# Kernel tuning notes

Measured on AMD Instinct MI355X. Metric: run time of the kernel, lower is better.

The kernel has to match this reference:

```python
import jax, jax.numpy as jnp
import numpy as np

N_NODES = 100000
N_EDGES = 3200000
IN_DIM, HID_DIM, OUT_DIM = 512, 256, 64


def setup_inputs() -> dict:
    key = jax.random.key(0)
    k1, k2, k3, k4, k5, k6 = jax.random.split(key, 6)
    x = jax.random.normal(k1, (N_NODES, IN_DIM), dtype=jnp.float32)
    src = jax.random.randint(k2, (N_EDGES,), 0, N_NODES, dtype=jnp.int32)
    dst = jax.random.randint(k3, (N_EDGES,), 0, N_NODES, dtype=jnp.int32)
    edge_index = jnp.stack([src, dst])  # [2, E]: row 0 = src (column), row 1 = dst (row)
    edge_weight = jax.random.uniform(k4, (N_EDGES,), dtype=jnp.float32)
    # Xavier-uniform init like nn.init.xavier_uniform_
    lim1 = float(np.sqrt(6.0 / (IN_DIM + HID_DIM)))
    lim2 = float(np.sqrt(6.0 / (HID_DIM + OUT_DIM)))
    W1 = jax.random.uniform(k5, (IN_DIM, HID_DIM), minval=-lim1, maxval=lim1, dtype=jnp.float32)
    W2 = jax.random.uniform(k6, (HID_DIM, OUT_DIM), minval=-lim2, maxval=lim2, dtype=jnp.float32)
    return {"x": x, "edge_index": edge_index, "edge_weight": edge_weight, "W1": W1, "W2": W2}


def _spmm(edge_index, edge_weight, support):
    # out[dst] += w * support[src]  (sparse adjacency @ dense support)
    src, dst = edge_index[0], edge_index[1]
    msgs = support[src] * edge_weight[:, None]  # [E, F]
    return jax.ops.segment_sum(msgs, dst, num_segments=N_NODES)


def reference(x, edge_index, edge_weight, W1, W2):
    # Layer 1: dense GEMM then SpMM, then ReLU (dropout is identity in eval)
    h = _spmm(edge_index, edge_weight, x @ W1)
    h = jax.nn.relu(h)
    # Layer 2
    out = _spmm(edge_index, edge_weight, h @ W2)
    return jax.nn.softmax(out, axis=1)
```

## Files before the change

### kernel.cpp

```cpp
#include <hip/hip_runtime.h>
#include <hip/hip_bf16.h>

typedef __attribute__((ext_vector_type(8))) short bf16x8;
typedef __attribute__((ext_vector_type(4))) float f32x4;
typedef __attribute__((ext_vector_type(8))) float f32x8;
typedef __attribute__((ext_vector_type(4))) _Float16 f16x4;
typedef __attribute__((ext_vector_type(8))) _Float16 f16x8;
typedef unsigned short ushort_t;

#define NN   100000
#define NE   3200000
#define IND  512
#define HIDD 256
#define OUTD 64

#define NBKT 98
#define P1E  2048
#define MPAN 782

__device__ __forceinline__ ushort_t f2bf(float a) {
    unsigned u = __float_as_uint(a);
    unsigned r = (u + 0x7FFFu + ((u >> 16) & 1u)) >> 16;
    return (ushort_t)r;
}
__device__ __forceinline__ float bf2f(ushort_t b) {
    return __uint_as_float(((unsigned)b) << 16);
}

union U8 { ushort_t us[8]; unsigned u32[4]; uint4 v; };

#define GLOAD_LDS16(gp, lp) \
    __builtin_amdgcn_global_load_lds( \
        (const __attribute__((address_space(1))) void*)(const void*)(gp), \
        (__attribute__((address_space(3))) void*)(void*)(lp), 16, 0, 0)

__device__ __forceinline__ void split8(float4 v0, float4 v1, bf16x8& aH, bf16x8& aL) {
    float vv[8] = {v0.x, v0.y, v0.z, v0.w, v1.x, v1.y, v1.z, v1.w};
    U8 H, L;
    #pragma unroll
    for (int j = 0; j < 4; ++j) {
        unsigned u0 = __float_as_uint(vv[2 * j]);
        unsigned u1 = __float_as_uint(vv[2 * j + 1]);
        H.u32[j] = __builtin_amdgcn_perm(u1, u0, 0x07060302u);
        float r0 = vv[2 * j]     - __uint_as_float(u0 & 0xFFFF0000u);
        float r1 = vv[2 * j + 1] - __uint_as_float(u1 & 0xFFFF0000u);
        L.u32[j] = __builtin_amdgcn_perm(__float_as_uint(r1),
                                         __float_as_uint(r0), 0x07060302u);
    }
    aH = *(const bf16x8*)&H.v;
    aL = *(const bf16x8*)&L.v;
}

__global__ void splitw_k(const float* __restrict__ in, ushort_t* __restrict__ thi,
                         ushort_t* __restrict__ tlo, int R, int C) {
    int i = blockIdx.x * 256 + threadIdx.x;
    if (i < R * C) {
        int r = i / C, c = i % C;
        float a = in[i];
        ushort_t h = f2bf(a);
        thi[(size_t)c * R + r] = h;
        tlo[(size_t)c * R + r] = f2bf(a - bf2f(h));
    }
}

__global__ __launch_bounds__(256, 3) void gemm1_k(
    const float* __restrict__ A, const ushort_t* __restrict__ BtHi,
    const ushort_t* __restrict__ BtLo, _Float16* __restrict__ C)
{
    const int M = NN, N = HIDD, K = IND;
    __shared__ __align__(16) float    sA [128 * 32];
    __shared__ __align__(16) ushort_t sBh[128 * 32];
    __shared__ __align__(16) ushort_t sBl[128 * 32];

    const int bid   = blockIdx.x;
    const int grp   = bid >> 4;
    const int rr_   = bid & 15;
    const int panel = grp * 8 + (rr_ & 7);
    if (panel >= MPAN) return;
    const int m0 = panel * 128;
    const int n0 = (rr_ >> 3) * 128;

    const int tid  = threadIdx.x;
    const int wave = tid >> 6;
    const int lane = tid & 63;
    const int quad = lane >> 4;
    const int l15  = lane & 15;
    const int wr   = wave >> 1;
    const int wc   = wave & 1;

    const float* aSrc[4];
    float*       aDst[4];
    #pragma unroll
    for (int it = 0; it < 4; ++it) {
        int f = it * 256 + tid;
        int r = f >> 3;
        int bp = (f & 7) ^ ((r & 3) << 1) ^ ((r >> 2) & 1);
        int gr = m0 + r; if (gr >= M) gr = M - 1;
        aSrc[it] = A + (size_t)gr * K + bp * 4;
        aDst[it] = &sA[f * 4];
    }
    const ushort_t* bhSrc[2]; const ushort_t* blSrc[2];
    ushort_t* bhDst[2]; ushort_t* blDst[2];
    #pragma unroll
    for (int it = 0; it < 2; ++it) {
        int f = it * 256 + tid;
        int r = f >> 2;
        int qp = (f & 3) ^ ((r >> 1) & 3);
        bhSrc[it] = BtHi + (size_t)(n0 + r) * K + qp * 8;
        blSrc[it] = BtLo + (size_t)(n0 + r) * K + qp * 8;
        bhDst[it] = &sBh[f * 8];
        blDst[it] = &sBl[f * 8];
    }

    int aOff[4][2];
    #pragma unroll
    for (int ms = 0; ms < 4; ++ms) {
        int rA = wr * 64 + ms * 16 + l15;
        int sw = ((rA & 3) << 1) ^ ((rA >> 2) & 1);
        int cb = quad << 1;
        aOff[ms][0] = rA * 32 + (((cb    ) ^ sw) << 2);
        aOff[ms][1] = rA * 32 + (((cb | 1) ^ sw) << 2);
    }
    int bOff[4];
    #pragma unroll
    for (int ns = 0; ns < 4; ++ns) {
        int rB = wc * 64 + ns * 16 + l15;
        bOff[ns] = rB * 32 + (quad ^ ((rB >> 1) & 3)) * 8;
    }

    f32x4 acc[4][4] = {};

    for (int k0 = 0; k0 < K; k0 += 32) {
        #pragma unroll
        for (int it = 0; it < 4; ++it) GLOAD_LDS16(aSrc[it] + k0, aDst[it]);
        #pragma unroll
        for (int it = 0; it < 2; ++it) {
            GLOAD_LDS16(bhSrc[it] + k0, bhDst[it]);
            GLOAD_LDS16(blSrc[it] + k0, blDst[it]);
        }
        __syncthreads();

        bf16x8 aH[4], aL[4];
        #pragma unroll
        for (int ms = 0; ms < 4; ++ms) {
            float4 v0 = *(const float4*)&sA[aOff[ms][0]];
            float4 v1 = *(const float4*)&sA[aOff[ms][1]];
            split8(v0, v1, aH[ms], aL[ms]);
        }

        #pragma unroll
        for (int ns = 0; ns < 4; ++ns) {
            bf16x8 bH = *(const bf16x8*)&sBh[bOff[ns]];
            bf16x8 bL = *(const bf16x8*)&sBl[bOff[ns]];
            #pragma unroll
            for (int ms = 0; ms < 4; ++ms) {
                acc[ms][ns] = __builtin_amdgcn_mfma_f32_16x16x32_bf16(aH[ms], bH, acc[ms][ns], 0, 0, 0);
                acc[ms][ns] = __builtin_amdgcn_mfma_f32_16x16x32_bf16(aL[ms], bH, acc[ms][ns], 0, 0, 0);
                acc[ms][ns] = __builtin_amdgcn_mfma_f32_16x16x32_bf16(aH[ms], bL, acc[ms][ns], 0, 0, 0);
            }
        }
        __syncthreads();
    }

    #pragma unroll
    for (int ms = 0; ms < 4; ++ms) {
        int row = m0 + wr * 64 + ms * 16 + quad * 4;
        #pragma unroll
        for (int ns = 0; ns < 4; ++ns) {
            int col = n0 + wc * 64 + ns * 16 + l15;
            #pragma unroll
            for (int r = 0; r < 4; ++r)
                if (row + r < M) C[(size_t)(row + r) * N + col] = (_Float16)acc[ms][ns][r];
        }
    }
}

__global__ __launch_bounds__(256) void bhist_k(const int* __restrict__ dst,
                                               int* __restrict__ bucketHist) {
    __shared__ int h[NBKT];
    int t = threadIdx.x;
    if (t < NBKT) h[t] = 0;
    __syncthreads();
    #pragma unroll
    for (int j = 0; j < 4; ++j) {
        int e = blockIdx.x * 1024 + t + j * 256;
        if (e < NE) atomicAdd(&h[dst[e] >> 10], 1);
    }
    __syncthreads();
    if (t < NBKT && h[t]) atomicAdd(&bucketHist[t], h[t]);
}

__global__ __launch_bounds__(128) void bscan_k(const int* __restrict__ bucketHist,
                                               int* __restrict__ bucketStart,
                                               int* __restrict__ bucketCursor) {
    __shared__ int s[128];
    int t = threadIdx.x;
    int v = (t < NBKT) ? bucketHist[t] : 0;
    s[t] = v;
    for (int off = 1; off < 128; off <<= 1) {
        __syncthreads();
        int a = (t >= off) ? s[t - off] : 0;
        __syncthreads();
        s[t] += a;
    }
    __syncthreads();
    if (t < NBKT) { bucketStart[t] = s[t] - v; bucketCursor[t] = s[t] - v; }
    if (t == NBKT - 1) bucketStart[NBKT] = s[t];
}

__global__ __launch_bounds__(256) void phase1_k(
    const int* __restrict__ src, const int* __restrict__ dst,
    const float* __restrict__ w, int* __restrict__ bucketCursor,
    int2* __restrict__ binned)
{
    __shared__ int2 raw[P1E];
    __shared__ int2 ord[P1E];
    __shared__ ushort_t rbkt[P1E], obkt[P1E];
    __shared__ int hist[128], excl[128], cursor[128], gbase[128], stmp[128];

    int t = threadIdx.x;
    if (t < 128) hist[t] = 0;
    __syncthreads();

    int e0 = blockIdx.x * P1E;
    #pragma unroll
    for (int j = 0; j < P1E / 256; ++j) {
        int li = t + j * 256;
        int e = e0 + li;
        if (e < NE) {
            int d = dst[e];
            int b = d >> 10;
            raw[li] = make_int2(src[e] | ((d & 1023) << 17), __float_as_int(w[e]));
            rbkt[li] = (ushort_t)b;
            atomicAdd(&hist[b], 1);
        } else rbkt[li] = 0xFFFFu;
    }
    __syncthreads();
    int v = (t < 128) ? hist[t] : 0;
    if (t < 128) stmp[t] = v;
    for (int off = 1; off < 128; off <<= 1) {
        __syncthreads();
        int a = (t < 128 && t >= off) ? stmp[t - off] : 0;
        __syncthreads();
        if (t < 128) stmp[t] += a;
    }
    __syncthreads();
    if (t < 128) { excl[t] = stmp[t] - v; cursor[t] = stmp[t] - v; }
    if (t < NBKT) gbase[t] = atomicAdd(&bucketCursor[t], hist[t]);
    __syncthreads();
    #pragma unroll
    for (int j = 0; j < P1E / 256; ++j) {
        int li = t + j * 256;
        ushort_t b = rbkt[li];
        if (b != 0xFFFFu) {
            int p = atomicAdd(&cursor[b], 1);
            ord[p] = raw[li];
            obkt[p] = b;
        }
    }
    __syncthreads();
    int tot = excl[NBKT - 1] + hist[NBKT - 1];
    #pragma unroll
    for (int j = 0; j < P1E / 256; ++j) {
        int li = t + j * 256;
        if (li < tot) {
            int b = obkt[li];
            binned[(size_t)gbase[b] + (li - excl[b])] = ord[li];
        }
    }
}

__global__ __launch_bounds__(256) void phase2_k(
    const int* __restrict__ bucketStart, const int2* __restrict__ binned,
    int* __restrict__ rowptr, int2* __restrict__ esw)
{
    __shared__ int cnt[1024], ex[1024], cur[1024], wsum[256];
    int t = threadIdx.x, blk = blockIdx.x;
    int gb = bucketStart[blk], ge = bucketStart[blk + 1];
    #pragma unroll
    for (int j = 0; j < 4; ++j) cnt[t + j * 256] = 0;
    __syncthreads();
    for (int e = gb + t; e < ge; e += 256)
        atomicAdd(&cnt[(binned[e].x >> 17) & 1023], 1);
    __syncthreads();
    int b4 = t * 4;
    int l0 = cnt[b4], l1 = cnt[b4 + 1], l2 = cnt[b4 + 2], l3 = cnt[b4 + 3];
    int ls = l0 + l1 + l2 + l3;
    wsum[t] = ls;
    for (int off = 1; off < 256; off <<= 1) {
        __syncthreads();
        int a = (t >= off) ? wsum[t - off] : 0;
        __syncthreads();
        wsum[t] += a;
    }
    __syncthreads();
    int be = wsum[t] - ls;
    ex[b4] = be;            cur[b4] = be;
    ex[b4 + 1] = be + l0;     cur[b4 + 1] = be + l0;
    ex[b4 + 2] = be + l0 + l1;  cur[b4 + 2] = be + l0 + l1;
    ex[b4 + 3] = be + l0 + l1 + l2; cur[b4 + 3] = be + l0 + l1 + l2;
    __syncthreads();
    int n0 = blk << 10;
    #pragma unroll
    for (int j = 0; j < 4; ++j) {
        int i = b4 + j;
        if (n0 + i < NN) rowptr[n0 + i] = gb + ex[i];
    }
    if (blk == NBKT - 1 && t == 0) rowptr[NN] = NE;
    for (int e = gb + t; e < ge; e += 256) {
        int2 en = binned[e];
        int d = (en.x >> 17) & 1023;
        int p = atomicAdd(&cur[d], 1);
        esw[(size_t)gb + p] = make_int2(en.x & 0x1FFFF, en.y);
    }
}

__global__ __launch_bounds__(256) void spmm_relu_gemm2_k(
    const int* __restrict__ rowptr, const int2* __restrict__ esw,
    const _Float16* __restrict__ X, const ushort_t* __restrict__ BtHi,
    const ushort_t* __restrict__ BtLo, _Float16* __restrict__ S2)
{
    __shared__ __align__(16) float h[16][260];

    const int wave  = threadIdx.x >> 6;
    const int lane  = threadIdx.x & 63;
    const int quad  = lane >> 4;
    const int l15   = lane & 15;
    const int half  = lane >> 5;
    const int l31   = lane & 31;
    const int nbase = blockIdx.x * 16;

    const _Float16* Xl = X + l31 * 8;
    #pragma unroll
    for (int i = 0; i < 4; ++i) {
        const int ln   = wave * 4 + i;
        const int node = nbase + ln;
        const int beg = rowptr[node], end = rowptr[node + 1];
        f32x8 acc = {0.f, 0.f, 0.f, 0.f, 0.f, 0.f, 0.f, 0.f};
        int e = beg;
        #pragma unroll 4
        for (; e + 1 < end; e += 2) {
            int2 sw = esw[e + half];
            float w = __int_as_float(sw.y);
            f16x8 v = *(const f16x8*)(Xl + (size_t)sw.x * HIDD);
            #pragma unroll
            for (int j = 0; j < 8; ++j) acc[j] += (float)v[j] * w;
        }
        if (e < end) {
            int2 sw = esw[e];
            float w = half ? 0.f : __int_as_float(sw.y);
            f16x8 v = *(const f16x8*)(Xl + (size_t)sw.x * HIDD);
            #pragma unroll
            for (int j = 0; j < 8; ++j) acc[j] += (float)v[j] * w;
        }
        #pragma unroll
        for (int j = 0; j < 8; ++j) acc[j] += __shfl_xor(acc[j], 32);
        if (half == 0) {
            float4 r0, r1;
            r0.x = fmaxf(acc[0], 0.f); r0.y = fmaxf(acc[1], 0.f);
            r0.z = fmaxf(acc[2], 0.f); r0.w = fmaxf(acc[3], 0.f);
            r1.x = fmaxf(acc[4], 0.f); r1.y = fmaxf(acc[5], 0.f);
            r1.z = fmaxf(acc[6], 0.f); r1.w = fmaxf(acc[7], 0.f);
            *(float4*)&h[ln][l31 * 8]     = r0;
            *(float4*)&h[ln][l31 * 8 + 4] = r1;
        }
    }
    __syncthreads();

    f32x4 acc2 = {0.f, 0.f, 0.f, 0.f};
    const ushort_t* bh = BtHi + (size_t)(wave * 16 + l15) * HIDD;
    const ushort_t* bl = BtLo + (size_t)(wave * 16 + l15) * HIDD;
    #pragma unroll
    for (int ks = 0; ks < 8; ++ks) {
        const int ko = ks * 32 + quad * 8;
        const float* ap = &h[l15][ko];
        float4 v0 = *(const float4*)ap;
        float4 v1 = *(const float4*)(ap + 4);
        bf16x8 aH, aL;
        split8(v0, v1, aH, aL);
        bf16x8 bH = *(const bf16x8*)(bh + ko);
        bf16x8 bL = *(const bf16x8*)(bl + ko);
        acc2 = __builtin_amdgcn_mfma_f32_16x16x32_bf16(aH, bH, acc2, 0, 0, 0);
        acc2 = __builtin_amdgcn_mfma_f32_16x16x32_bf16(aL, bH, acc2, 0, 0, 0);
        acc2 = __builtin_amdgcn_mfma_f32_16x16x32_bf16(aH, bL, acc2, 0, 0, 0);
    }
    #pragma unroll
    for (int r = 0; r < 4; ++r) {
        const int node = nbase + quad * 4 + r;
        S2[(size_t)node * OUTD + wave * 16 + l15] = (_Float16)acc2[r];
    }
}

__global__ __launch_bounds__(256) void spmm_softmax_k(
    const int* __restrict__ rowptr, const int2* __restrict__ esw,
    const _Float16* __restrict__ X, float* __restrict__ out)
{
    const int node = blockIdx.x * 4 + (threadIdx.x >> 6);
    const int lane = threadIdx.x & 63;
    const int g    = lane >> 4;
    const int l15  = lane & 15;
    const int beg = rowptr[node], end = rowptr[node + 1];

    f32x4 acc = {0.f, 0.f, 0.f, 0.f};
    const _Float16* Xl = X + l15 * 4;
    int e = beg;
    #pragma unroll 4
    for (; e + 3 < end; e += 4) {
        int2 sw = esw[e + g];
        float w = __int_as_float(sw.y);
        f16x4 v = *(const f16x4*)(Xl + (size_t)sw.x * OUTD);
        acc.x += (float)v[0] * w;
        acc.y += (float)v[1] * w;
        acc.z += (float)v[2] * w;
        acc.w += (float)v[3] * w;
    }
    if (e < end) {
        int idx = e + g;
        int2 sw = esw[min(idx, end - 1)];
        float w = (idx < end) ? __int_as_float(sw.y) : 0.f;
        f16x4 v = *(const f16x4*)(Xl + (size_t)sw.x * OUTD);
        acc.x += (float)v[0] * w;
        acc.y += (float)v[1] * w;
        acc.z += (float)v[2] * w;
        acc.w += (float)v[3] * w;
    }
    acc.x += __shfl_xor(acc.x, 16); acc.x += __shfl_xor(acc.x, 32);
    acc.y += __shfl_xor(acc.y, 16); acc.y += __shfl_xor(acc.y, 32);
    acc.z += __shfl_xor(acc.z, 16); acc.z += __shfl_xor(acc.z, 32);
    acc.w += __shfl_xor(acc.w, 16); acc.w += __shfl_xor(acc.w, 32);

    float mx = fmaxf(fmaxf(acc.x, acc.y), fmaxf(acc.z, acc.w));
    #pragma unroll
    for (int off = 8; off > 0; off >>= 1) mx = fmaxf(mx, __shfl_xor(mx, off));
    float e0 = __expf(acc.x - mx), e1 = __expf(acc.y - mx);
    float e2 = __expf(acc.z - mx), e3 = __expf(acc.w - mx);
    float sm = e0 + e1 + e2 + e3;
    #pragma unroll
    for (int off = 8; off > 0; off >>= 1) sm += __shfl_xor(sm, off);
    if (g == 0) {
        float inv = 1.f / sm;
        f32x4 r = {e0 * inv, e1 * inv, e2 * inv, e3 * inv};
        *(f32x4*)(out + (size_t)node * OUTD + l15 * 4) = r;
    }
}

extern "C" void kernel_launch(void* const* d_in, const int* in_sizes, int n_in,
                              void* d_out, int out_size, void* d_ws, size_t ws_size,
                              hipStream_t stream) {
    const float* x  = (const float*)d_in[0];
    const int*   ei = (const int*)d_in[1];
    const float* ew = (const float*)d_in[2];
    const float* W1 = (const float*)d_in[3];
    const float* W2 = (const float*)d_in[4];
    float* out = (float*)d_out;
    const int* src = ei;
    const int* dst = ei + NE;

    char* ws = (char*)d_ws;
    size_t o = 0;
    auto take = [&](size_t bytes) -> void* {
        void* p = (void*)(ws + o);
        o += (bytes + 255) & ~(size_t)255;
        return p;
    };
    _Float16* S1      = (_Float16*)take((size_t)NN * HIDD * 2);
    _Float16* S2      = (_Float16*)take((size_t)NN * OUTD * 2);
    int2*     binned  = (int2*    )take((size_t)NE * 8);
    ushort_t* W1tHi   = (ushort_t*)take((size_t)IND * HIDD * 2);
    ushort_t* W1tLo   = (ushort_t*)take((size_t)IND * HIDD * 2);
    ushort_t* W2tHi   = (ushort_t*)take((size_t)HIDD * OUTD * 2);
    ushort_t* W2tLo   = (ushort_t*)take((size_t)HIDD * OUTD * 2);
    int*      rowptr  = (int*     )take((size_t)(NN + 1) * 4);
    int*      bHist   = (int*     )take(NBKT * 4);
    int*      bStart  = (int*     )take((NBKT + 1) * 4);
    int*      bCursor = (int*     )take(NBKT * 4);
    int2*     esw     = (int2*    )take((size_t)NE * 8);
    (void)in_sizes; (void)n_in; (void)out_size; (void)ws_size;

    hipMemsetAsync(bHist, 0, NBKT * 4, stream);
    splitw_k<<<(IND * HIDD + 255) / 256, 256, 0, stream>>>(W1, W1tHi, W1tLo, IND, HIDD);
    splitw_k<<<(HIDD * OUTD + 255) / 256, 256, 0, stream>>>(W2, W2tHi, W2tLo, HIDD, OUTD);

    bhist_k<<<(NE + 1023) / 1024, 256, 0, stream>>>(dst, bHist);
    bscan_k<<<1, 128, 0, stream>>>(bHist, bStart, bCursor);
    phase1_k<<<(NE + P1E - 1) / P1E, 256, 0, stream>>>(src, dst, ew, bCursor, binned);
    phase2_k<<<NBKT, 256, 0, stream>>>(bStart, binned, rowptr, esw);

    const int G1 = ((MPAN + 7) / 8) * 16;
    gemm1_k<<<G1, 256, 0, stream>>>(x, W1tHi, W1tLo, S1);
    spmm_relu_gemm2_k<<<NN / 16, 256, 0, stream>>>(rowptr, esw, S1, W2tHi, W2tLo, S2);
    spmm_softmax_k<<<NN / 4, 256, 0, stream>>>(rowptr, esw, S2, out);
}
```

Baseline: 828.0 us.

## Double-buffer A tile in GEMM1, read B directly from global, unroll SpMM loops

The GEMM1 kernel now double-buffers the A tile in shared memory, prefetching the next K slice while computing on the current one. The B hi/lo fragments are loaded straight from global memory (L2-resident weights) instead of being staged through LDS. This drops one barrier per iteration and overlaps the A loads with compute. The SpMM loops also get a larger unroll factor to keep more gathers in flight. Direct global B reads add latency inside the MFMA loop, and the larger unrolls raise register pressure.

```diff
diff --git a/kernel.cpp b/kernel.cpp
--- a/kernel.cpp
+++ b/kernel.cpp
@@ -68,9 +68,7 @@
     const ushort_t* __restrict__ BtLo, _Float16* __restrict__ C)
 {
     const int M = NN, N = HIDD, K = IND;
-    __shared__ __align__(16) float    sA [128 * 32];
-    __shared__ __align__(16) ushort_t sBh[128 * 32];
-    __shared__ __align__(16) ushort_t sBl[128 * 32];
+    __shared__ __align__(16) float sA[2][128 * 32];
 
     const int bid   = blockIdx.x;
     const int grp   = bid >> 4;
@@ -89,7 +87,7 @@
     const int wc   = wave & 1;
 
     const float* aSrc[4];
-    float*       aDst[4];
+    int aDstOff[4];
     #pragma unroll
     for (int it = 0; it < 4; ++it) {
         int f = it * 256 + tid;
@@ -97,19 +95,14 @@
         int bp = (f & 7) ^ ((r & 3) << 1) ^ ((r >> 2) & 1);
         int gr = m0 + r; if (gr >= M) gr = M - 1;
         aSrc[it] = A + (size_t)gr * K + bp * 4;
-        aDst[it] = &sA[f * 4];
-    }
-    const ushort_t* bhSrc[2]; const ushort_t* blSrc[2];
-    ushort_t* bhDst[2]; ushort_t* blDst[2];
-    #pragma unroll
-    for (int it = 0; it < 2; ++it) {
-        int f = it * 256 + tid;
-        int r = f >> 2;
-        int qp = (f & 3) ^ ((r >> 1) & 3);
-        bhSrc[it] = BtHi + (size_t)(n0 + r) * K + qp * 8;
-        blSrc[it] = BtLo + (size_t)(n0 + r) * K + qp * 8;
-        bhDst[it] = &sBh[f * 8];
-        blDst[it] = &sBl[f * 8];
+        aDstOff[it] = f * 4;
+    }
+    const ushort_t* bhp[4]; const ushort_t* blp[4];
+    #pragma unroll
+    for (int ns = 0; ns < 4; ++ns) {
+        int rB = n0 + wc * 64 + ns * 16 + l15;
+        bhp[ns] = BtHi + (size_t)rB * K + quad * 8;
+        blp[ns] = BtLo + (size_t)rB * K + quad * 8;
     }
 
     int aOff[4][2];
@@ -121,37 +114,33 @@
         aOff[ms][0] = rA * 32 + (((cb    ) ^ sw) << 2);
         aOff[ms][1] = rA * 32 + (((cb | 1) ^ sw) << 2);
     }
-    int bOff[4];
-    #pragma unroll
-    for (int ns = 0; ns < 4; ++ns) {
-        int rB = wc * 64 + ns * 16 + l15;
-        bOff[ns] = rB * 32 + (quad ^ ((rB >> 1) & 3)) * 8;
-    }
 
     f32x4 acc[4][4] = {};
 
+    #pragma unroll
+    for (int it = 0; it < 4; ++it) GLOAD_LDS16(aSrc[it], &sA[0][aDstOff[it]]);
+    __syncthreads();
+
+    int cur = 0;
     for (int k0 = 0; k0 < K; k0 += 32) {
-        #pragma unroll
-        for (int it = 0; it < 4; ++it) GLOAD_LDS16(aSrc[it] + k0, aDst[it]);
-        #pragma unroll
-        for (int it = 0; it < 2; ++it) {
-            GLOAD_LDS16(bhSrc[it] + k0, bhDst[it]);
-            GLOAD_LDS16(blSrc[it] + k0, blDst[it]);
-        }
-        __syncthreads();
+        if (k0 + 32 < K) {
+            #pragma unroll
+            for (int it = 0; it < 4; ++it)
+                GLOAD_LDS16(aSrc[it] + k0 + 32, &sA[cur ^ 1][aDstOff[it]]);
+        }
 
         bf16x8 aH[4], aL[4];
         #pragma unroll
         for (int ms = 0; ms < 4; ++ms) {
-            float4 v0 = *(const float4*)&sA[aOff[ms][0]];
-            float4 v1 = *(const float4*)&sA[aOff[ms][1]];
+            float4 v0 = *(const float4*)&sA[cur][aOff[ms][0]];
+            float4 v1 = *(const float4*)&sA[cur][aOff[ms][1]];
             split8(v0, v1, aH[ms], aL[ms]);
         }
 
         #pragma unroll
         for (int ns = 0; ns < 4; ++ns) {
-            bf16x8 bH = *(const bf16x8*)&sBh[bOff[ns]];
-            bf16x8 bL = *(const bf16x8*)&sBl[bOff[ns]];
+            bf16x8 bH = *(const bf16x8*)(bhp[ns] + k0);
+            bf16x8 bL = *(const bf16x8*)(blp[ns] + k0);
             #pragma unroll
             for (int ms = 0; ms < 4; ++ms) {
                 acc[ms][ns] = __builtin_amdgcn_mfma_f32_16x16x32_bf16(aH[ms], bH, acc[ms][ns], 0, 0, 0);
@@ -160,6 +149,7 @@
             }
         }
         __syncthreads();
+        cur ^= 1;
     }
 
     #pragma unroll
@@ -338,7 +328,7 @@
         const int beg = rowptr[node], end = rowptr[node + 1];
         f32x8 acc = {0.f, 0.f, 0.f, 0.f, 0.f, 0.f, 0.f, 0.f};
         int e = beg;
-        #pragma unroll 4
+        #pragma unroll 8
         for (; e + 1 < end; e += 2) {
             int2 sw = esw[e + half];
             float w = __int_as_float(sw.y);
@@ -404,7 +394,7 @@
     f32x4 acc = {0.f, 0.f, 0.f, 0.f};
     const _Float16* Xl = X + l15 * 4;
     int e = beg;
-    #pragma unroll 4
+    #pragma unroll 8
     for (; e + 3 < end; e += 4) {
         int2 sw = esw[e + g];
         float w = __int_as_float(sw.y);
```

Result: slower. 941.5 us (+13.7%).
